# Kernel tuning notes

Measured on AMD Instinct MI355X. Metric: run time of the kernel, lower is better.

The kernel has to match this reference:

```python
import jax, jax.numpy as jnp
import numpy as np


def setup_inputs() -> dict:
    key = jax.random.key(0)
    kq, kk, kv = jax.random.split(key, 3)
    B, S, H, D = 2, 2048, 16, 64
    q = jax.random.normal(kq, (B, S, H, D), dtype=jnp.float32)
    k = jax.random.normal(kk, (B, S, H, D), dtype=jnp.float32)
    v = jax.random.normal(kv, (B, S, H, D), dtype=jnp.float32)
    # additive key padding mask, [B,1,1,K]; 0 = unmasked, -inf = masked
    key_padding_mask = jnp.zeros((B, 1, 1, S), dtype=jnp.float32)
    return {"q": q, "k": k, "v": v, "key_padding_mask": key_padding_mask}


def reference(q, k, v, key_padding_mask):
    # q,k,v: [B, S, H, D]; key_padding_mask: [B,1,1,K] additive
    head_dim = q.shape[-1]
    softmax_scale = 1.0 / np.sqrt(head_dim).astype(np.float32)
    # [B, H, Q, K] logits with additive mask
    logits = jnp.einsum('bqhd,bkhd->bhqk', q, k) * softmax_scale + key_padding_mask
    attn = jax.nn.softmax(logits, axis=-1)
    # dropout p=0.0 -> identity in eval mode
    out = jnp.einsum('bhqk,bkhd->bqhd', attn, v)
    return out
```

## Files before the change

### kernel.cpp

```cpp
#include <hip/hip_runtime.h>
#include <hip/hip_bf16.h>


typedef __attribute__((ext_vector_type(8))) short bf16x8;
typedef __attribute__((ext_vector_type(4))) short bf16x4;
typedef __attribute__((ext_vector_type(4))) float f32x4;

#define B_ 2
#define S_ 2048
#define H_ 16
#define D_ 64
#define BQ 128
#define BK 64
#define NT (S_ / BK)
#define LDK 72
#define ROWSZ (H_ * D_)

#define LOG2E  1.44269504088896340736f
#define SCALE2 (0.125f * LOG2E)

__device__ __forceinline__ unsigned pack2(float a, float b) {
    union { __hip_bfloat162 h; unsigned u; } x;
    x.h = __float22bfloat162_rn(make_float2(a, b));
    return x.u;
}

__device__ __forceinline__ float fexp2(float x) {
#if __has_builtin(__builtin_amdgcn_exp2f)
    return __builtin_amdgcn_exp2f(x);
#else
    return __expf(x * 0.69314718055994531f);
#endif
}

__device__ __forceinline__ f32x4 mfma16(bf16x4 a, bf16x4 b, f32x4 c) {
#if __has_builtin(__builtin_amdgcn_mfma_f32_16x16x16bf16_1k)
    return __builtin_amdgcn_mfma_f32_16x16x16bf16_1k(a, b, c, 0, 0, 0);
#else
    bf16x8 a8 = {a[0], a[1], a[2], a[3], 0, 0, 0, 0};
    bf16x8 b8 = {b[0], b[1], b[2], b[3], 0, 0, 0, 0};
    return __builtin_amdgcn_mfma_f32_16x16x32_bf16(a8, b8, c, 0, 0, 0);
#endif
}

__global__ __launch_bounds__(512, 4)
void fattn_kernel(const float* __restrict__ qg,
                  const float* __restrict__ kg,
                  const float* __restrict__ vg,
                  const float* __restrict__ maskg,
                  float* __restrict__ outg)
{
    __shared__ __attribute__((aligned(16))) ushort Ks[2][BK * LDK];
    __shared__ __attribute__((aligned(16))) ushort Vt[2][D_ * LDK];
    __shared__ __attribute__((aligned(16))) float  Em[S_];

    const int qt = blockIdx.x, h = blockIdx.y, b = blockIdx.z;
    const int tid = threadIdx.x;
    const int w = tid >> 6, lane = tid & 63, g = lane >> 4, l15 = lane & 15;
    const int gh = g >> 1, glo = g & 1, h3 = l15 >> 3;

    {
        float4 mv = *(const float4*)(maskg + (size_t)b * S_ + tid * 4);
        *(float4*)&Em[tid * 4] = make_float4(mv.x * LOG2E, mv.y * LOG2E,
                                             mv.z * LOG2E, mv.w * LOG2E);
    }

    const int qrow = qt * BQ + w * 16 + l15;
    const float* qp = qg + (size_t)(b * S_ + qrow) * ROWSZ + h * D_;
    bf16x8 qf[2];
#pragma unroll
    for (int half = 0; half < 2; ++half) {
        float4 f0 = *(const float4*)(qp + half * 32 + g * 8);
        float4 f1 = *(const float4*)(qp + half * 32 + g * 8 + 4);
        union { bf16x8 v; uint4 u; } x;
        x.u = make_uint4(pack2(f0.x * SCALE2, f0.y * SCALE2),
                         pack2(f0.z * SCALE2, f0.w * SCALE2),
                         pack2(f1.x * SCALE2, f1.y * SCALE2),
                         pack2(f1.z * SCALE2, f1.w * SCALE2));
        qf[half] = x.v;
    }

    const int skey16 = tid >> 4;
    const int sd4    = (tid & 15) * 4;
    const int svd    = lane;
    const int svk8   = w * 8;
    const int vphys  = (w ^ ((lane >> 3) & 7)) * 8;

    const size_t kvbase = (size_t)b * S_ * ROWSZ + h * D_;

    float4 kpre0, kpre1;
    float  vpre[8];
    auto prefetch = [&](int kt) {
        const float* kb = kg + kvbase + (size_t)kt * BK * ROWSZ;
        kpre0 = *(const float4*)(kb + (size_t)skey16 * ROWSZ + sd4);
        kpre1 = *(const float4*)(kb + (size_t)(skey16 + 32) * ROWSZ + sd4);
        const float* vb = vg + kvbase + (size_t)kt * BK * ROWSZ + svd;
#pragma unroll
        for (int i = 0; i < 8; ++i) vpre[i] = vb[(size_t)(svk8 + i) * ROWSZ];
    };
    auto stage = [&](int buf) {
        *(uint2*)&Ks[buf][skey16 * LDK + sd4] =
            make_uint2(pack2(kpre0.x, kpre0.y), pack2(kpre0.z, kpre0.w));
        *(uint2*)&Ks[buf][(skey16 + 32) * LDK + sd4] =
            make_uint2(pack2(kpre1.x, kpre1.y), pack2(kpre1.z, kpre1.w));
        *(uint4*)&Vt[buf][svd * LDK + vphys] =
            make_uint4(pack2(vpre[0], vpre[1]), pack2(vpre[2], vpre[3]),
                       pack2(vpre[4], vpre[5]), pack2(vpre[6], vpre[7]));
    };

    float l_r = 0.0f;
    f32x4 o_acc[4];
#pragma unroll
    for (int t = 0; t < 4; ++t) o_acc[t] = (f32x4){0.f, 0.f, 0.f, 0.f};

    prefetch(0);
    stage(0);
    __syncthreads();

    const int koff  = l15 * LDK + g * 8;
    const int vbase = l15 * LDK + glo * 4;

    for (int kt = 0; kt < NT; ++kt) {
        const int cur = kt & 1;
        if (kt + 1 < NT) prefetch(kt + 1);

        const ushort* ks = Ks[cur];
        float sv[4][4];
#pragma unroll
        for (int t = 0; t < 4; ++t) {
            f32x4 acc = *(const f32x4*)&Em[kt * BK + t * 16 + g * 4];
            bf16x8 kf0 = *(const bf16x8*)&ks[t * 16 * LDK + koff];
            bf16x8 kf1 = *(const bf16x8*)&ks[t * 16 * LDK + koff + 32];
            acc = __builtin_amdgcn_mfma_f32_16x16x32_bf16(kf0, qf[0], acc, 0, 0, 0);
            acc = __builtin_amdgcn_mfma_f32_16x16x32_bf16(kf1, qf[1], acc, 0, 0, 0);
            sv[t][0] = acc[0]; sv[t][1] = acc[1]; sv[t][2] = acc[2]; sv[t][3] = acc[3];
        }

        float rs = 0.f;
#pragma unroll
        for (int t = 0; t < 4; ++t)
#pragma unroll
            for (int r = 0; r < 4; ++r) {
                float p = fexp2(sv[t][r]);
                sv[t][r] = p;
                rs += p;
            }
        l_r += rs;

        bf16x4 pf[4];
#pragma unroll
        for (int c = 0; c < 4; ++c) {
            union { bf16x4 v; uint2 u; } x;
            x.u = make_uint2(pack2(sv[c][0], sv[c][1]), pack2(sv[c][2], sv[c][3]));
            pf[c] = x.v;
        }

        const ushort* vt = Vt[cur];
#pragma unroll
        for (int t2 = 0; t2 < 4; ++t2) {
            const int e = (2 * t2 + h3) & 7;
#pragma unroll
            for (int c = 0; c < 4; ++c) {
                const int physu = (2 * c + gh) ^ e;
                bf16x4 vf = *(const bf16x4*)&vt[t2 * 16 * LDK + vbase + physu * 8];
                o_acc[t2] = mfma16(vf, pf[c], o_acc[t2]);
            }
        }

        if (kt + 1 < NT) stage(cur ^ 1);
        __syncthreads();
    }

    l_r += __shfl_xor(l_r, 16);
    l_r += __shfl_xor(l_r, 32);
    const float inv = 1.0f / l_r;
    float* op = outg + (size_t)(b * S_ + qrow) * ROWSZ + h * D_;
#pragma unroll
    for (int t2 = 0; t2 < 4; ++t2)
#pragma unroll
        for (int r = 0; r < 4; ++r)
            op[t2 * 16 + g * 4 + r] = o_acc[t2][r] * inv;
}

extern "C" void kernel_launch(void* const* d_in, const int* in_sizes, int n_in,
                              void* d_out, int out_size, void* d_ws, size_t ws_size,
                              hipStream_t stream) {
    dim3 grid(S_ / BQ, H_, B_);
    fattn_kernel<<<grid, dim3(512), 0, stream>>>(
        (const float*)d_in[0], (const float*)d_in[1], (const float*)d_in[2],
        (const float*)d_in[3], (float*)d_out);
}
```

Before: 145.7 us.

## Software-pipeline QK of next tile with softmax/PV of current using triple buffering

Restructures the main loop so the QK^T MFMAs for tile kt+1 are interleaved with the exp and PV MFMAs of tile kt, using three LDS buffers and ping-pong score registers. Global prefetch now runs two tiles ahead. The aim is to hide exp/VALU latency behind matrix work and overlap the memory loads more deeply. It costs extra LDS and extra registers for the second score array, which may lower occupancy under launch_bounds(512,4).

```diff
diff --git a/kernel.cpp b/kernel.cpp
--- a/kernel.cpp
+++ b/kernel.cpp
@@ -50,8 +50,8 @@
                   const float* __restrict__ maskg,
                   float* __restrict__ outg)
 {
-    __shared__ __attribute__((aligned(16))) ushort Ks[2][BK * LDK];
-    __shared__ __attribute__((aligned(16))) ushort Vt[2][D_ * LDK];
+    __shared__ __attribute__((aligned(16))) ushort Ks[3][BK * LDK];
+    __shared__ __attribute__((aligned(16))) ushort Vt[3][D_ * LDK];
     __shared__ __attribute__((aligned(16))) float  Em[S_];
 
     const int qt = blockIdx.x, h = blockIdx.y, b = blockIdx.z;
@@ -113,62 +113,61 @@
 #pragma unroll
     for (int t = 0; t < 4; ++t) o_acc[t] = (f32x4){0.f, 0.f, 0.f, 0.f};
 
-    prefetch(0);
-    stage(0);
-    __syncthreads();
-
     const int koff  = l15 * LDK + g * 8;
     const int vbase = l15 * LDK + glo * 4;
 
-    for (int kt = 0; kt < NT; ++kt) {
-        const int cur = kt & 1;
-        if (kt + 1 < NT) prefetch(kt + 1);
+    auto qkchunk = [&](int kt, int buf, int c, float (&sv)[4][4]) {
+        f32x4 acc = *(const f32x4*)&Em[kt * BK + c * 16 + g * 4];
+        const ushort* ks = Ks[buf];
+        bf16x8 kf0 = *(const bf16x8*)&ks[c * 16 * LDK + koff];
+        bf16x8 kf1 = *(const bf16x8*)&ks[c * 16 * LDK + koff + 32];
+        acc = __builtin_amdgcn_mfma_f32_16x16x32_bf16(kf0, qf[0], acc, 0, 0, 0);
+        acc = __builtin_amdgcn_mfma_f32_16x16x32_bf16(kf1, qf[1], acc, 0, 0, 0);
+        sv[c][0] = acc[0]; sv[c][1] = acc[1]; sv[c][2] = acc[2]; sv[c][3] = acc[3];
+    };
 
-        const ushort* ks = Ks[cur];
-        float sv[4][4];
+    float svA[4][4], svB[4][4];
+
+    prefetch(0); stage(0);
+    prefetch(1);
+    __syncthreads();
 #pragma unroll
-        for (int t = 0; t < 4; ++t) {
-            f32x4 acc = *(const f32x4*)&Em[kt * BK + t * 16 + g * 4];
-            bf16x8 kf0 = *(const bf16x8*)&ks[t * 16 * LDK + koff];
-            bf16x8 kf1 = *(const bf16x8*)&ks[t * 16 * LDK + koff + 32];
-            acc = __builtin_amdgcn_mfma_f32_16x16x32_bf16(kf0, qf[0], acc, 0, 0, 0);
-            acc = __builtin_amdgcn_mfma_f32_16x16x32_bf16(kf1, qf[1], acc, 0, 0, 0);
-            sv[t][0] = acc[0]; sv[t][1] = acc[1]; sv[t][2] = acc[2]; sv[t][3] = acc[3];
-        }
+    for (int c = 0; c < 4; ++c) qkchunk(0, 0, c, svA);
+    stage(1);
+    prefetch(2);
+    __syncthreads();
 
+    auto body = [&](int kt, float (&scur)[4][4], float (&snxt)[4][4]) {
+        const int bcur = kt % 3, bnxt = (kt + 1) % 3, bstg = (kt + 2) % 3;
+        const ushort* vt = Vt[bcur];
+        const bool do_next = (kt + 1 < NT);
         float rs = 0.f;
 #pragma unroll
-        for (int t = 0; t < 4; ++t)
+        for (int c = 0; c < 4; ++c) {
+            float p0 = fexp2(scur[c][0]), p1 = fexp2(scur[c][1]);
+            float p2 = fexp2(scur[c][2]), p3 = fexp2(scur[c][3]);
+            rs += (p0 + p1) + (p2 + p3);
+            union { bf16x4 v; uint2 u; } x;
+            x.u = make_uint2(pack2(p0, p1), pack2(p2, p3));
+            const bf16x4 pfc = x.v;
+            if (do_next) qkchunk(kt + 1, bnxt, c, snxt);
 #pragma unroll
-            for (int r = 0; r < 4; ++r) {
-                float p = fexp2(sv[t][r]);
-                sv[t][r] = p;
-                rs += p;
-            }
-        l_r += rs;
-
-        bf16x4 pf[4];
-#pragma unroll
-        for (int c = 0; c < 4; ++c) {
-            union { bf16x4 v; uint2 u; } x;
-            x.u = make_uint2(pack2(sv[c][0], sv[c][1]), pack2(sv[c][2], sv[c][3]));
-            pf[c] = x.v;
-        }
-
-        const ushort* vt = Vt[cur];
-#pragma unroll
-        for (int t2 = 0; t2 < 4; ++t2) {
-            const int e = (2 * t2 + h3) & 7;
-#pragma unroll
-            for (int c = 0; c < 4; ++c) {
+            for (int t2 = 0; t2 < 4; ++t2) {
+                const int e = (2 * t2 + h3) & 7;
                 const int physu = (2 * c + gh) ^ e;
                 bf16x4 vf = *(const bf16x4*)&vt[t2 * 16 * LDK + vbase + physu * 8];
-                o_acc[t2] = mfma16(vf, pf[c], o_acc[t2]);
+                o_acc[t2] = mfma16(vf, pfc, o_acc[t2]);
             }
         }
+        l_r += rs;
+        if (kt + 2 < NT) stage(bstg);
+        if (kt + 3 < NT) prefetch(kt + 3);
+        if (kt + 1 < NT) __syncthreads();
+    };
 
-        if (kt + 1 < NT) stage(cur ^ 1);
-        __syncthreads();
+    for (int k2 = 0; k2 < NT; k2 += 2) {
+        body(k2,     svA, svB);
+        body(k2 + 1, svB, svA);
     }
 
     l_r += __shfl_xor(l_r, 16);
```

New measurement: 157.1 us. +7.9%, slower.

## Pre-convert K/V to swizzled bf16 tiles and stream via global_load_lds

Applied to the files above, without the earlier changes.

Adds two pre-pass kernels that convert K to bf16 in a swizzled tiled layout and V to a transposed swizzled bf16 layout in workspace. The attention kernel then loads each tile straight into LDS with 16-byte global_load_lds, removing per-block fp32 loads, conversion and LDS staging from the main loop. The mask is now read from global memory each tile instead of being staged in LDS. This costs two extra launches and a full extra pass over K and V, which is amortized over the 16 query tiles that reuse them. The original kernel is kept as a fallback when the workspace is too small.

```diff
diff --git a/kernel.cpp b/kernel.cpp
--- a/kernel.cpp
+++ b/kernel.cpp
@@ -43,27 +43,81 @@
 #endif
 }
 
+__device__ __forceinline__ void gll16(const ushort* g, ushort* l) {
+    __builtin_amdgcn_global_load_lds(
+        (const __attribute__((address_space(1))) void*)g,
+        (__attribute__((address_space(3))) void*)l, 16, 0, 0);
+}
+
+__global__ __launch_bounds__(256)
+void prep_k(const float* __restrict__ kg, ushort* __restrict__ kb) {
+    const int cid  = blockIdx.x * 256 + threadIdx.x;
+    const int phys = cid & 511;
+    const int tile = cid >> 9;
+    const int key  = phys >> 3;
+    const int dc   = (phys & 7) ^ (key & 7);
+    const int kt   = tile & (NT - 1);
+    const int bh   = tile >> 5;
+    const int h    = bh & (H_ - 1);
+    const int b    = bh >> 4;
+    const float* src = kg + ((size_t)(b * S_ + kt * BK + key) * H_ + h) * D_ + dc * 8;
+    float4 f0 = *(const float4*)src;
+    float4 f1 = *(const float4*)(src + 4);
+    ((uint4*)kb)[cid] = make_uint4(pack2(f0.x, f0.y), pack2(f0.z, f0.w),
+                                   pack2(f1.x, f1.y), pack2(f1.z, f1.w));
+}
+
+__global__ __launch_bounds__(256)
+void prep_v(const float* __restrict__ vg, ushort* __restrict__ vb) {
+    __shared__ ushort T[BK][80];
+    const int tile = blockIdx.x;
+    const int kt = tile & (NT - 1);
+    const int bh = tile >> 5;
+    const int h  = bh & (H_ - 1);
+    const int b  = bh >> 4;
+    const int t  = threadIdx.x;
+    {
+        const int key = t >> 2, d0 = (t & 3) * 16;
+        const float* src = vg + ((size_t)(b * S_ + kt * BK + key) * H_ + h) * D_ + d0;
+        float4 a0 = *(const float4*)(src);
+        float4 a1 = *(const float4*)(src + 4);
+        float4 a2 = *(const float4*)(src + 8);
+        float4 a3 = *(const float4*)(src + 12);
+        *(uint4*)&T[key][d0]     = make_uint4(pack2(a0.x, a0.y), pack2(a0.z, a0.w),
+                                              pack2(a1.x, a1.y), pack2(a1.z, a1.w));
+        *(uint4*)&T[key][d0 + 8] = make_uint4(pack2(a2.x, a2.y), pack2(a2.z, a2.w),
+                                              pack2(a3.x, a3.y), pack2(a3.z, a3.w));
+    }
+    __syncthreads();
+    const size_t obase = (size_t)bh * D_ * (S_ / 8);
+#pragma unroll
+    for (int i = 0; i < 2; ++i) {
+        const int c = 2 * t + i;
+        const int d = c >> 3, slot = c & 7;
+        const int k0 = (slot ^ (d & 7)) * 8;
+        unsigned p0 = (unsigned)T[k0 + 0][d] | ((unsigned)T[k0 + 1][d] << 16);
+        unsigned p1 = (unsigned)T[k0 + 2][d] | ((unsigned)T[k0 + 3][d] << 16);
+        unsigned p2 = (unsigned)T[k0 + 4][d] | ((unsigned)T[k0 + 5][d] << 16);
+        unsigned p3 = (unsigned)T[k0 + 6][d] | ((unsigned)T[k0 + 7][d] << 16);
+        ((uint4*)vb)[obase + (size_t)d * (S_ / 8) + kt * 8 + slot] =
+            make_uint4(p0, p1, p2, p3);
+    }
+}
+
 __global__ __launch_bounds__(512, 4)
-void fattn_kernel(const float* __restrict__ qg,
-                  const float* __restrict__ kg,
-                  const float* __restrict__ vg,
-                  const float* __restrict__ maskg,
-                  float* __restrict__ outg)
+void fattn_gll(const float* __restrict__ qg,
+               const ushort* __restrict__ kb,
+               const ushort* __restrict__ vb,
+               const float* __restrict__ maskg,
+               float* __restrict__ outg)
 {
-    __shared__ __attribute__((aligned(16))) ushort Ks[2][BK * LDK];
-    __shared__ __attribute__((aligned(16))) ushort Vt[2][D_ * LDK];
-    __shared__ __attribute__((aligned(16))) float  Em[S_];
+    __shared__ __attribute__((aligned(16))) ushort Ks[2][BK * D_];
+    __shared__ __attribute__((aligned(16))) ushort Vt[2][D_ * BK];
 
     const int qt = blockIdx.x, h = blockIdx.y, b = blockIdx.z;
     const int tid = threadIdx.x;
     const int w = tid >> 6, lane = tid & 63, g = lane >> 4, l15 = lane & 15;
-    const int gh = g >> 1, glo = g & 1, h3 = l15 >> 3;
-
-    {
-        float4 mv = *(const float4*)(maskg + (size_t)b * S_ + tid * 4);
-        *(float4*)&Em[tid * 4] = make_float4(mv.x * LOG2E, mv.y * LOG2E,
-                                             mv.z * LOG2E, mv.w * LOG2E);
-    }
+    const int gh = g >> 1, glo = g & 1, e7 = l15 & 7;
 
     const int qrow = qt * BQ + w * 16 + l15;
     const float* qp = qg + (size_t)(b * S_ + qrow) * ROWSZ + h * D_;
@@ -80,23 +134,132 @@
         qf[half] = x.v;
     }
 
+    const ushort* ktile0 = kb + (size_t)((b * H_ + h) * NT) * (BK * D_)
+                              + (size_t)(w * 64 + lane) * 8;
+    const ushort* vrow0  = vb + ((size_t)(b * H_ + h) * D_ + (w * 8 + (lane >> 3))) * S_
+                              + (lane & 7) * 8;
+    const float* maskb = maskg + (size_t)b * S_;
+
+    float l_r = 0.0f;
+    f32x4 o_acc[4];
+#pragma unroll
+    for (int t = 0; t < 4; ++t) o_acc[t] = (f32x4){0.f, 0.f, 0.f, 0.f};
+
+    gll16(ktile0, &Ks[0][w * 512]);
+    gll16(vrow0,  &Vt[0][w * 512]);
+    __syncthreads();
+
+    for (int kt = 0; kt < NT; ++kt) {
+        const int cur = kt & 1;
+        if (kt + 1 < NT) {
+            gll16(ktile0 + (size_t)(kt + 1) * (BK * D_), &Ks[cur ^ 1][w * 512]);
+            gll16(vrow0  + (size_t)(kt + 1) * 64,        &Vt[cur ^ 1][w * 512]);
+        }
+
+        const ushort* ks = Ks[cur];
+        float sv[4][4];
+#pragma unroll
+        for (int t = 0; t < 4; ++t) {
+            const int rb = (t * 16 + l15) * 64;
+            bf16x8 kf0 = *(const bf16x8*)&ks[rb + ((g       ^ e7) * 8)];
+            bf16x8 kf1 = *(const bf16x8*)&ks[rb + (((g + 4) ^ e7) * 8)];
+            f32x4 acc = (f32x4){0.f, 0.f, 0.f, 0.f};
+            acc = __builtin_amdgcn_mfma_f32_16x16x32_bf16(kf0, qf[0], acc, 0, 0, 0);
+            acc = __builtin_amdgcn_mfma_f32_16x16x32_bf16(kf1, qf[1], acc, 0, 0, 0);
+            sv[t][0] = acc[0]; sv[t][1] = acc[1]; sv[t][2] = acc[2]; sv[t][3] = acc[3];
+        }
+
+        float rs = 0.f;
+        bf16x4 pf[4];
+#pragma unroll
+        for (int t = 0; t < 4; ++t) {
+            const f32x4 mk = *(const f32x4*)(maskb + kt * BK + t * 16 + g * 4);
+            float p0 = fexp2(fmaf(mk[0], LOG2E, sv[t][0]));
+            float p1 = fexp2(fmaf(mk[1], LOG2E, sv[t][1]));
+            float p2 = fexp2(fmaf(mk[2], LOG2E, sv[t][2]));
+            float p3 = fexp2(fmaf(mk[3], LOG2E, sv[t][3]));
+            rs += (p0 + p1) + (p2 + p3);
+            union { bf16x4 v; uint2 u; } x;
+            x.u = make_uint2(pack2(p0, p1), pack2(p2, p3));
+            pf[t] = x.v;
+        }
+        l_r += rs;
+
+        const ushort* vt = Vt[cur];
+#pragma unroll
+        for (int t2 = 0; t2 < 4; ++t2) {
+            const int rb = (t2 * 16 + l15) * 64;
+#pragma unroll
+            for (int c = 0; c < 4; ++c) {
+                const int s = (2 * c + gh) ^ e7;
+                bf16x4 vf = *(const bf16x4*)&vt[rb + s * 8 + glo * 4];
+                o_acc[t2] = mfma16(vf, pf[c], o_acc[t2]);
+            }
+        }
+
+        __syncthreads();
+    }
+
+    l_r += __shfl_xor(l_r, 16);
+    l_r += __shfl_xor(l_r, 32);
+    const float inv = 1.0f / l_r;
+    float* op = outg + (size_t)(b * S_ + qrow) * ROWSZ + h * D_;
+#pragma unroll
+    for (int t2 = 0; t2 < 4; ++t2)
+#pragma unroll
+        for (int r = 0; r < 4; ++r)
+            op[t2 * 16 + g * 4 + r] = o_acc[t2][r] * inv;
+}
+
+__global__ __launch_bounds__(512, 4)
+void fattn_fb(const float* __restrict__ qg,
+              const float* __restrict__ kg,
+              const float* __restrict__ vg,
+              const float* __restrict__ maskg,
+              float* __restrict__ outg)
+{
+    __shared__ __attribute__((aligned(16))) ushort Ks[2][BK * LDK];
+    __shared__ __attribute__((aligned(16))) ushort Vt[2][D_ * LDK];
+    __shared__ __attribute__((aligned(16))) float  Em[S_];
+
+    const int qt = blockIdx.x, h = blockIdx.y, b = blockIdx.z;
+    const int tid = threadIdx.x;
+    const int w = tid >> 6, lane = tid & 63, g = lane >> 4, l15 = lane & 15;
+    const int gh = g >> 1, glo = g & 1, h3 = l15 >> 3;
+    {
+        float4 mv = *(const float4*)(maskg + (size_t)b * S_ + tid * 4);
+        *(float4*)&Em[tid * 4] = make_float4(mv.x * LOG2E, mv.y * LOG2E,
+                                             mv.z * LOG2E, mv.w * LOG2E);
+    }
+    const int qrow = qt * BQ + w * 16 + l15;
+    const float* qp = qg + (size_t)(b * S_ + qrow) * ROWSZ + h * D_;
+    bf16x8 qf[2];
+#pragma unroll
+    for (int half = 0; half < 2; ++half) {
+        float4 f0 = *(const float4*)(qp + half * 32 + g * 8);
+        float4 f1 = *(const float4*)(qp + half * 32 + g * 8 + 4);
+        union { bf16x8 v; uint4 u; } x;
+        x.u = make_uint4(pack2(f0.x * SCALE2, f0.y * SCALE2),
+                         pack2(f0.z * SCALE2, f0.w * SCALE2),
+                         pack2(f1.x * SCALE2, f1.y * SCALE2),
+                         pack2(f1.z * SCALE2, f1.w * SCALE2));
+        qf[half] = x.v;
+    }
     const int skey16 = tid >> 4;
     const int sd4    = (tid & 15) * 4;
     const int svd    = lane;
     const int svk8   = w * 8;
     const int vphys  = (w ^ ((lane >> 3) & 7)) * 8;
-
     const size_t kvbase = (size_t)b * S_ * ROWSZ + h * D_;
-
     float4 kpre0, kpre1;
     float  vpre[8];
     auto prefetch = [&](int kt) {
-        const float* kb = kg + kvbase + (size_t)kt * BK * ROWSZ;
-        kpre0 = *(const float4*)(kb + (size_t)skey16 * ROWSZ + sd4);
-        kpre1 = *(const float4*)(kb + (size_t)(skey16 + 32) * ROWSZ + sd4);
-        const float* vb = vg + kvbase + (size_t)kt * BK * ROWSZ + svd;
-#pragma unroll
-        for (int i = 0; i < 8; ++i) vpre[i] = vb[(size_t)(svk8 + i) * ROWSZ];
+        const float* kbp = kg + kvbase + (size_t)kt * BK * ROWSZ;
+        kpre0 = *(const float4*)(kbp + (size_t)skey16 * ROWSZ + sd4);
+        kpre1 = *(const float4*)(kbp + (size_t)(skey16 + 32) * ROWSZ + sd4);
+        const float* vbp = vg + kvbase + (size_t)kt * BK * ROWSZ + svd;
+#pragma unroll
+        for (int i = 0; i < 8; ++i) vpre[i] = vbp[(size_t)(svk8 + i) * ROWSZ];
     };
     auto stage = [&](int buf) {
         *(uint2*)&Ks[buf][skey16 * LDK + sd4] =
@@ -107,23 +270,18 @@
             make_uint4(pack2(vpre[0], vpre[1]), pack2(vpre[2], vpre[3]),
                        pack2(vpre[4], vpre[5]), pack2(vpre[6], vpre[7]));
     };
-
     float l_r = 0.0f;
     f32x4 o_acc[4];
 #pragma unroll
     for (int t = 0; t < 4; ++t) o_acc[t] = (f32x4){0.f, 0.f, 0.f, 0.f};
-
     prefetch(0);
     stage(0);
     __syncthreads();
-
     const int koff  = l15 * LDK + g * 8;
     const int vbase = l15 * LDK + glo * 4;
-
     for (int kt = 0; kt < NT; ++kt) {
         const int cur = kt & 1;
         if (kt + 1 < NT) prefetch(kt + 1);
-
         const ushort* ks = Ks[cur];
         float sv[4][4];
 #pragma unroll
@@ -135,7 +293,6 @@
             acc = __builtin_amdgcn_mfma_f32_16x16x32_bf16(kf1, qf[1], acc, 0, 0, 0);
             sv[t][0] = acc[0]; sv[t][1] = acc[1]; sv[t][2] = acc[2]; sv[t][3] = acc[3];
         }
-
         float rs = 0.f;
 #pragma unroll
         for (int t = 0; t < 4; ++t)
@@ -146,7 +303,6 @@
                 rs += p;
             }
         l_r += rs;
-
         bf16x4 pf[4];
 #pragma unroll
         for (int c = 0; c < 4; ++c) {
@@ -154,7 +310,6 @@
             x.u = make_uint2(pack2(sv[c][0], sv[c][1]), pack2(sv[c][2], sv[c][3]));
             pf[c] = x.v;
         }
-
         const ushort* vt = Vt[cur];
 #pragma unroll
         for (int t2 = 0; t2 < 4; ++t2) {
@@ -166,11 +321,9 @@
                 o_acc[t2] = mfma16(vf, pf[c], o_acc[t2]);
             }
         }
-
         if (kt + 1 < NT) stage(cur ^ 1);
         __syncthreads();
     }
-
     l_r += __shfl_xor(l_r, 16);
     l_r += __shfl_xor(l_r, 32);
     const float inv = 1.0f / l_r;
@@ -185,8 +338,23 @@
 extern "C" void kernel_launch(void* const* d_in, const int* in_sizes, int n_in,
                               void* d_out, int out_size, void* d_ws, size_t ws_size,
                               hipStream_t stream) {
+    const float* q    = (const float*)d_in[0];
+    const float* k    = (const float*)d_in[1];
+    const float* v    = (const float*)d_in[2];
+    const float* mask = (const float*)d_in[3];
+    float* out = (float*)d_out;
+
+    const size_t elems = (size_t)B_ * H_ * S_ * D_;
+    const size_t need  = elems * sizeof(ushort) * 2;
     dim3 grid(S_ / BQ, H_, B_);
-    fattn_kernel<<<grid, dim3(512), 0, stream>>>(
-        (const float*)d_in[0], (const float*)d_in[1], (const float*)d_in[2],
-        (const float*)d_in[3], (float*)d_out);
-}
+
+    if (ws_size >= need) {
+        ushort* kbuf = (ushort*)d_ws;
+        ushort* vbuf = kbuf + elems;
+        prep_k<<<2048, 256, 0, stream>>>(k, kbuf);
+        prep_v<<<1024, 256, 0, stream>>>(v, vbuf);
+        fattn_gll<<<grid, dim3(512), 0, stream>>>(q, kbuf, vbuf, mask, out);
+    } else {
+        fattn_fb<<<grid, dim3(512), 0, stream>>>(q, k, v, mask, out);
+    }
+}
```

New measurement: 159.3 us. 9.4% more time.
